# Kernel optimization log

Hardware: AMD Instinct MI355X
Metric: run time of the kernel (lower is better)

The kernel has to match this reference:

```python
import jax, jax.numpy as jnp
import numpy as np

STRIDE = (1, 1, 1)
PAD = (1, 1, 1)
CPG = 8  # channel_per_group


def setup_inputs() -> dict:
    key = jax.random.key(0)
    k1, k2, k3 = jax.random.split(key, 3)
    x = jax.random.normal(k1, (1, 64, 8, 56, 56), jnp.float32)
    offset = jax.random.normal(k2, (1, 648, 8, 56, 56), jnp.float32)
    n = 64 * 3 * 3 * 3
    stdv = 1.0 / np.sqrt(n)
    weight = jax.random.uniform(k3, (64, 64, 3, 3, 3), jnp.float32, -stdv, stdv)
    return {"x": x, "offset": offset, "weight": weight}


def _deform_conv3d(x, offset, weight, stride, padding, cpg):
    B, C, D, H, W = x.shape
    O, _, kD, kH, kW = weight.shape
    KV = kD * kH * kW
    G = C // cpg
    Do = (D + 2 * padding[0] - kD) // stride[0] + 1
    Ho = (H + 2 * padding[1] - kH) // stride[1] + 1
    Wo = (W + 2 * padding[2] - kW) // stride[2] + 1

    # offsets: [B, G, KV, 3(z,y,x), Do, Ho, Wo]
    off = offset.reshape(B, G, KV, 3, Do, Ho, Wo)

    f32 = x.dtype
    kz, ky, kx = jnp.meshgrid(jnp.arange(kD), jnp.arange(kH), jnp.arange(kW), indexing='ij')
    kz = kz.reshape(-1).astype(f32); ky = ky.reshape(-1).astype(f32); kx = kx.reshape(-1).astype(f32)
    oz = (jnp.arange(Do) * stride[0] - padding[0]).astype(f32)
    oy = (jnp.arange(Ho) * stride[1] - padding[1]).astype(f32)
    ox = (jnp.arange(Wo) * stride[2] - padding[2]).astype(f32)

    # sampling coords, broadcast to [B, G, KV, Do, Ho, Wo]
    zc = kz[None, None, :, None, None, None] + oz[None, None, None, :, None, None] + off[:, :, :, 0]
    yc = ky[None, None, :, None, None, None] + oy[None, None, None, None, :, None] + off[:, :, :, 1]
    xc = kx[None, None, :, None, None, None] + ox[None, None, None, None, None, :] + off[:, :, :, 2]

    z0 = jnp.floor(zc); y0 = jnp.floor(yc); x0 = jnp.floor(xc)
    dz = zc - z0; dy = yc - y0; dx = xc - x0
    z0i = z0.astype(jnp.int32); y0i = y0.astype(jnp.int32); x0i = x0.astype(jnp.int32)

    # channels-last grouped view: [B, G, D, H, W, cpg]
    xg = x.reshape(B, G, cpg, D, H, W).transpose(0, 1, 3, 4, 5, 2)
    bi = jnp.arange(B).reshape(B, 1, 1, 1, 1, 1)
    gi = jnp.arange(G).reshape(1, G, 1, 1, 1, 1)

    def gather(zi, yi, xi):
        valid = ((zi >= 0) & (zi < D) & (yi >= 0) & (yi < H) & (xi >= 0) & (xi < W))
        zcl = jnp.clip(zi, 0, D - 1)
        ycl = jnp.clip(yi, 0, H - 1)
        xcl = jnp.clip(xi, 0, W - 1)
        v = xg[bi, gi, zcl, ycl, xcl]  # [B,G,KV,Do,Ho,Wo,cpg]
        return v * valid.astype(f32)[..., None]

    val = jnp.zeros((B, G, KV, Do, Ho, Wo, cpg), f32)
    for zi, wz in ((z0i, 1.0 - dz), (z0i + 1, dz)):
        for yi, wy in ((y0i, 1.0 - dy), (y0i + 1, dy)):
            for xi, wx in ((x0i, 1.0 - dx), (x0i + 1, dx)):
                val = val + gather(zi, yi, xi) * (wz * wy * wx)[..., None]

    # [B,G,KV,Do,Ho,Wo,cpg] -> [B, C, KV, N]
    val = val.transpose(0, 1, 6, 2, 3, 4, 5).reshape(B, C, KV, Do * Ho * Wo)
    wmat = weight.reshape(O, C, KV)
    out = jnp.einsum('bckn,ock->bon', val, wmat)
    return out.reshape(B, O, Do, Ho, Wo)


def reference(x, offset, weight):
    return _deform_conv3d(x, offset, weight, STRIDE, PAD, CPG)
```

## Files before the change

kernel.cpp:

```cpp
#include <hip/hip_runtime.h>
#include <hip/hip_fp16.h>

namespace {
constexpr int D_ = 8, H_ = 56, W_ = 56;
constexpr int HW_ = H_ * W_;
constexpr int KV_ = 27;
constexpr int N_ = D_ * H_ * W_;
constexpr int NT_ = 16;
constexpr int NTILES_ = N_ / NT_;
}

typedef _Float16 f16x8 __attribute__((ext_vector_type(8)));
typedef float f32x4 __attribute__((ext_vector_type(4)));

union U4H { uint4 u; __half2 h[4]; f16x8 v; };

__global__ __launch_bounds__(256) void prep_kernel(const float* __restrict__ x,
                                                   const float* __restrict__ w,
                                                   __half* __restrict__ xt,
                                                   __half* __restrict__ wt2) {
    const int b = blockIdx.x, tid = threadIdx.x;
    if (b < 784) {
        const int g = b / 98;
        const int n = (b % 98) * 256 + tid;
        U4H p;
#pragma unroll
        for (int cc = 0; cc < 4; ++cc) {
            float lo = x[(size_t)(g * 8 + 2 * cc) * N_ + n];
            float hi = x[(size_t)(g * 8 + 2 * cc + 1) * N_ + n];
            p.h[cc] = __floats2half2_rn(lo, hi);
        }
        *(uint4*)(xt + ((size_t)g * N_ + n) * 8) = p.u;
    } else {
        const int idx = (b - 784) * 256 + tid;
        const int e  = idx & 7;
        const int l  = (idx >> 3) & 63;
        const int ks = (idx >> 9) & 1;
        const int of = (idx >> 10) & 3;
        const int kv = idx >> 12;
        const int o = of * 16 + (l & 15);
        const int c = ks * 32 + (l >> 4) * 8 + e;
        wt2[idx] = __float2half(w[(size_t)(o * 64 + c) * 27 + kv]);
    }
}

#define CORN(DU, WF, A) do {                                                   \
    U4H d_; d_.u = (DU);                                                       \
    __half2 w2_ = __float2half2_rn(WF);                                        \
    A.h[0] = __hfma2(d_.h[0], w2_, A.h[0]);                                    \
    A.h[1] = __hfma2(d_.h[1], w2_, A.h[1]);                                    \
    A.h[2] = __hfma2(d_.h[2], w2_, A.h[2]);                                    \
    A.h[3] = __hfma2(d_.h[3], w2_, A.h[3]);                                    \
} while (0)

__global__ __launch_bounds__(512, 4) void gather_kernel(const float* __restrict__ offset,
                                                        const __half* __restrict__ xt,
                                                        __half* __restrict__ val) {
    __shared__ uint4 lds_x[8 * 10 * 56];
    const int b2 = (blockIdx.x & 7) * 84 + (blockIdx.x >> 3);
    const int g = b2 / 84;
    const int r = b2 % 84;
    const int ys = (r / 3) * 2;
    const int kvt = r % 3;
    const int tid = threadIdx.x;

    const int ylo = max(0, ys - 4);
    const int yhi = min(55, ys + 5);
    const int Yw = yhi - ylo + 1;

    const uint4* xs = (const uint4*)(xt + (size_t)g * (N_ * 8));

    {
        const int tot = 8 * Yw * 56;
        for (int i = tid; i < tot; i += 512) {
            int z = i / (Yw * 56);
            int rem = i - z * (Yw * 56);
            int yy = rem / 56;
            int x = rem - yy * 56;
            lds_x[(z * 10 + yy) * 56 + x] = xs[z * HW_ + (ylo + yy) * 56 + x];
        }
    }
    __syncthreads();

    const float* obase = offset + (size_t)g * (KV_ * 3 * N_);
    const int kz = kvt;

    for (int s = tid; s < 8064; s += 512) {
        const int kvi = s / 896;
        const int p = s - kvi * 896;
        const int z = p / 112;
        const int rem = p - z * 112;
        const int yrow = rem / 56;
        const int x = rem - yrow * 56;
        const int y = ys + yrow;
        const int n = z * HW_ + y * W_ + x;
        const int kv = kvt * 9 + kvi;
        const int ky = kvi / 3, kx = kvi - ky * 3;

        const float* pofs = obase + (size_t)(kv * 3) * N_ + n;
        const float oz = __builtin_nontemporal_load(pofs);
        const float oy = __builtin_nontemporal_load(pofs + N_);
        const float ox = __builtin_nontemporal_load(pofs + 2 * N_);

        float zc = (float)(z + kz - 1) + oz;
        float yc = (float)(y + ky - 1) + oy;
        float xc = (float)(x + kx - 1) + ox;
        float zf = floorf(zc), yf = floorf(yc), xf = floorf(xc);
        float dz = zc - zf, dy = yc - yf, dx = xc - xf;
        int z0 = (int)zf, y0 = (int)yf, x0 = (int)xf;
        int z1 = z0 + 1, y1 = y0 + 1, x1 = x0 + 1;
        float wz0 = (1.f - dz) * ((unsigned)z0 < (unsigned)D_ ? 1.f : 0.f);
        float wz1 = dz * ((unsigned)z1 < (unsigned)D_ ? 1.f : 0.f);
        float wy0 = (1.f - dy) * ((unsigned)y0 < (unsigned)H_ ? 1.f : 0.f);
        float wy1 = dy * ((unsigned)y1 < (unsigned)H_ ? 1.f : 0.f);
        float wx0 = (1.f - dx) * ((unsigned)x0 < (unsigned)W_ ? 1.f : 0.f);
        float wx1 = dx * ((unsigned)x1 < (unsigned)W_ ? 1.f : 0.f);
        int z0c = min(max(z0, 0), D_ - 1), z1c = min(max(z1, 0), D_ - 1);
        int y0c = min(max(y0, 0), H_ - 1), y1c = min(max(y1, 0), H_ - 1);
        int x0c = min(max(x0, 0), W_ - 1), x1c = min(max(x1, 0), W_ - 1);

        uint4 c0, c1, c2, c3, c4, c5, c6, c7;
        const bool inw = (y0c >= ylo) && (y1c <= yhi);
        if (inw) {
            const int r00 = (z0c * 10 + (y0c - ylo)) * 56;
            const int r01 = (z0c * 10 + (y1c - ylo)) * 56;
            const int r10 = (z1c * 10 + (y0c - ylo)) * 56;
            const int r11 = (z1c * 10 + (y1c - ylo)) * 56;
            c0 = lds_x[r00 + x0c]; c1 = lds_x[r00 + x1c];
            c2 = lds_x[r01 + x0c]; c3 = lds_x[r01 + x1c];
            c4 = lds_x[r10 + x0c]; c5 = lds_x[r10 + x1c];
            c6 = lds_x[r11 + x0c]; c7 = lds_x[r11 + x1c];
        } else {
            const int zy00 = z0c * HW_ + y0c * W_, zy01 = z0c * HW_ + y1c * W_;
            const int zy10 = z1c * HW_ + y0c * W_, zy11 = z1c * HW_ + y1c * W_;
            c0 = xs[zy00 + x0c]; c1 = xs[zy00 + x1c];
            c2 = xs[zy01 + x0c]; c3 = xs[zy01 + x1c];
            c4 = xs[zy10 + x0c]; c5 = xs[zy10 + x1c];
            c6 = xs[zy11 + x0c]; c7 = xs[zy11 + x1c];
        }

        U4H a0, a1;
        a0.u = make_uint4(0u, 0u, 0u, 0u);
        a1.u = make_uint4(0u, 0u, 0u, 0u);
        float wzy00 = wz0 * wy0, wzy01 = wz0 * wy1;
        float wzy10 = wz1 * wy0, wzy11 = wz1 * wy1;
        CORN(c0, wzy00 * wx0, a0); CORN(c1, wzy00 * wx1, a1);
        CORN(c2, wzy01 * wx0, a0); CORN(c3, wzy01 * wx1, a1);
        CORN(c4, wzy10 * wx0, a0); CORN(c5, wzy10 * wx1, a1);
        CORN(c6, wzy11 * wx0, a0); CORN(c7, wzy11 * wx1, a1);
        a0.h[0] = __hadd2(a0.h[0], a1.h[0]);
        a0.h[1] = __hadd2(a0.h[1], a1.h[1]);
        a0.h[2] = __hadd2(a0.h[2], a1.h[2]);
        a0.h[3] = __hadd2(a0.h[3], a1.h[3]);

        const size_t didx = ((size_t)(kv * NTILES_ + (n >> 4)) << 10) + g * 128 + (n & 15) * 8;
        *(uint4*)(val + didx) = a0.u;
    }
}

__global__ __launch_bounds__(256, 4) void gemm_kernel(const __half* __restrict__ val,
                                                      const __half* __restrict__ wt2,
                                                      float* __restrict__ out) {
    __shared__ float red_s[4][64][20];
    const int tid = threadIdx.x, lane = tid & 63, wv = tid >> 6;
    const int nt = blockIdx.x;
    const int n0 = nt * NT_, nl = lane & 15;
    const int kv0 = wv * 7;
    f32x4 acc[4] = {};
    const __half* vb = val + (size_t)nt * 1024 + lane * 8;
    const __half* wb0 = wt2 + lane * 8;
#pragma unroll
    for (int t = 0; t < 7; ++t) {
        const int kv = kv0 + t;
        if (kv < KV_) {
            const __half* vp = vb + (size_t)kv * (NTILES_ * 1024);
            f16x8 bf0 = *(const f16x8*)(vp);
            f16x8 bf1 = *(const f16x8*)(vp + 512);
            const __half* wb = wb0 + (size_t)kv * 4096;
            f16x8 a00 = *(const f16x8*)(wb);
            f16x8 a01 = *(const f16x8*)(wb + 1024);
            f16x8 a02 = *(const f16x8*)(wb + 2048);
            f16x8 a03 = *(const f16x8*)(wb + 3072);
            acc[0] = __builtin_amdgcn_mfma_f32_16x16x32_f16(a00, bf0, acc[0], 0, 0, 0);
            acc[1] = __builtin_amdgcn_mfma_f32_16x16x32_f16(a01, bf0, acc[1], 0, 0, 0);
            acc[2] = __builtin_amdgcn_mfma_f32_16x16x32_f16(a02, bf0, acc[2], 0, 0, 0);
            acc[3] = __builtin_amdgcn_mfma_f32_16x16x32_f16(a03, bf0, acc[3], 0, 0, 0);
            f16x8 a10 = *(const f16x8*)(wb + 512);
            f16x8 a11 = *(const f16x8*)(wb + 1536);
            f16x8 a12 = *(const f16x8*)(wb + 2560);
            f16x8 a13 = *(const f16x8*)(wb + 3584);
            acc[0] = __builtin_amdgcn_mfma_f32_16x16x32_f16(a10, bf1, acc[0], 0, 0, 0);
            acc[1] = __builtin_amdgcn_mfma_f32_16x16x32_f16(a11, bf1, acc[1], 0, 0, 0);
            acc[2] = __builtin_amdgcn_mfma_f32_16x16x32_f16(a12, bf1, acc[2], 0, 0, 0);
            acc[3] = __builtin_amdgcn_mfma_f32_16x16x32_f16(a13, bf1, acc[3], 0, 0, 0);
        }
    }
#pragma unroll
    for (int of = 0; of < 4; ++of)
#pragma unroll
        for (int rr = 0; rr < 4; ++rr)
            red_s[wv][of * 16 + (lane >> 4) * 4 + rr][nl] = acc[of][rr];
    __syncthreads();
    const int o = tid >> 2, n4 = (tid & 3) * 4;
    f32x4 s = *(const f32x4*)&red_s[0][o][n4] + *(const f32x4*)&red_s[1][o][n4]
            + *(const f32x4*)&red_s[2][o][n4] + *(const f32x4*)&red_s[3][o][n4];
    *(f32x4*)(out + (size_t)o * N_ + n0 + n4) = s;
}

#define ISSUE(PH, KY, KX, OZ, OY, OX, BUF, WW) do {                            \
    float zc = (float)(zo + kz - 1) + (OZ);                                    \
    float yc = (float)(yo + (KY) - 1) + (OY);                                  \
    float xc = (float)(xo + (KX) - 1) + (OX);                                  \
    float zf = floorf(zc), yf = floorf(yc), xf = floorf(xc);                   \
    float dz = zc - zf, dy = yc - yf, dx = xc - xf;                            \
    int z0 = (int)zf, y0 = (int)yf, x0 = (int)xf;                              \
    int z1 = z0 + 1, y1 = y0 + 1, x1 = x0 + 1;                                 \
    WW[0] = (1.f - dz) * ((unsigned)z0 < (unsigned)D_ ? 1.f : 0.f);            \
    WW[1] = dz * ((unsigned)z1 < (unsigned)D_ ? 1.f : 0.f);                    \
    WW[2] = (1.f - dy) * ((unsigned)y0 < (unsigned)H_ ? 1.f : 0.f);            \
    WW[3] = dy * ((unsigned)y1 < (unsigned)H_ ? 1.f : 0.f);                    \
    WW[4] = (1.f - dx) * ((unsigned)x0 < (unsigned)W_ ? 1.f : 0.f);            \
    WW[5] = dx * ((unsigned)x1 < (unsigned)W_ ? 1.f : 0.f);                    \
    int z0c = min(max(z0, 0), D_ - 1), z1c = min(max(z1, 0), D_ - 1);          \
    int y0c = min(max(y0, 0), H_ - 1), y1c = min(max(y1, 0), H_ - 1);          \
    int x0c = min(max(x0, 0), W_ - 1), x1c = min(max(x1, 0), W_ - 1);          \
    const uint4* xp_ = xg[PH];                                                 \
    int zy00 = z0c * HW_ + y0c * W_, zy01 = z0c * HW_ + y1c * W_;              \
    int zy10 = z1c * HW_ + y0c * W_, zy11 = z1c * HW_ + y1c * W_;              \
    BUF[0] = xp_[zy00 + x0c]; BUF[1] = xp_[zy00 + x1c];                        \
    BUF[2] = xp_[zy01 + x0c]; BUF[3] = xp_[zy01 + x1c];                        \
    BUF[4] = xp_[zy10 + x0c]; BUF[5] = xp_[zy10 + x1c];                        \
    BUF[6] = xp_[zy11 + x0c]; BUF[7] = xp_[zy11 + x1c];                        \
} while (0)

#define CONSUME(BUF, WW, BF) do {                                              \
    U4H a0_, a1_;                                                              \
    a0_.u = make_uint4(0u, 0u, 0u, 0u);                                        \
    a1_.u = make_uint4(0u, 0u, 0u, 0u);                                        \
    float wzy00 = WW[0] * WW[2], wzy01 = WW[0] * WW[3];                        \
    float wzy10 = WW[1] * WW[2], wzy11 = WW[1] * WW[3];                        \
    CORN(BUF[0], wzy00 * WW[4], a0_); CORN(BUF[1], wzy00 * WW[5], a1_);        \
    CORN(BUF[2], wzy01 * WW[4], a0_); CORN(BUF[3], wzy01 * WW[5], a1_);        \
    CORN(BUF[4], wzy10 * WW[4], a0_); CORN(BUF[5], wzy10 * WW[5], a1_);        \
    CORN(BUF[6], wzy11 * WW[4], a0_); CORN(BUF[7], wzy11 * WW[5], a1_);        \
    a0_.h[0] = __hadd2(a0_.h[0], a1_.h[0]);                                    \
    a0_.h[1] = __hadd2(a0_.h[1], a1_.h[1]);                                    \
    a0_.h[2] = __hadd2(a0_.h[2], a1_.h[2]);                                    \
    a0_.h[3] = __hadd2(a0_.h[3], a1_.h[3]);                                    \
    BF = a0_.v;                                                                \
} while (0)

__global__ __launch_bounds__(192, 3) void dconv_kernel(const float* __restrict__ offset,
                                                       const __half* __restrict__ xt,
                                                       const __half* __restrict__ wt2,
                                                       float* __restrict__ out) {
    __shared__ float red_s[3][64][20];
    const int tid = threadIdx.x;
    const int lane = tid & 63;
    const int wv = tid >> 6;
    const int r = blockIdx.x;
    const int tile = (r & 7) * 196 + (r >> 3);
    const int n0 = tile * NT_;
    const int nl = lane & 15;
    const int n = n0 + nl;
    const int kv0 = wv * 9;
    const int kz = wv;

    const int zo = n / HW_;
    const int rem = n - zo * HW_;
    const int yo = rem / W_;
    const int xo = rem - yo * W_;
    const uint4* xg[2];
    const float* ob[2];
#pragma unroll
    for (int ph = 0; ph < 2; ++ph) {
        const int g = ph * 4 + (lane >> 4);
        xg[ph] = (const uint4*)(xt + (size_t)g * (N_ * 8));
        ob[ph] = offset + (size_t)g * (KV_ * 3 * N_) + n;
    }

    uint4 bufA[8], bufB[8];
    float wA[6], wB[6];
    f32x4 acc[4] = {};
    f16x8 bf0, bf1;

    float o0z[2], o0y[2], o0x[2], onz[2], ony[2], onx[2];
#pragma unroll
    for (int ph = 0; ph < 2; ++ph) {
        const float* p = ob[ph] + (size_t)kv0 * 3 * N_;
        o0z[ph] = __builtin_nontemporal_load(p);
        o0y[ph] = __builtin_nontemporal_load(p + N_);
        o0x[ph] = __builtin_nontemporal_load(p + 2 * N_);
    }
    ISSUE(0, 0, 0, o0z[0], o0y[0], o0x[0], bufA, wA);
    ISSUE(1, 0, 0, o0z[1], o0y[1], o0x[1], bufB, wB);
#pragma unroll
    for (int ph = 0; ph < 2; ++ph) {
        const float* p = ob[ph] + (size_t)(kv0 + 1) * 3 * N_;
        onz[ph] = __builtin_nontemporal_load(p);
        ony[ph] = __builtin_nontemporal_load(p + N_);
        onx[ph] = __builtin_nontemporal_load(p + 2 * N_);
    }

#pragma unroll
    for (int t = 0; t < 9; ++t) {
        const int kv = kv0 + t;
        const __half* wb = wt2 + (size_t)kv * 4096 + lane * 8;
        f16x8 af00 = *(const f16x8*)(wb);
        f16x8 af01 = *(const f16x8*)(wb + 1024);
        f16x8 af02 = *(const f16x8*)(wb + 2048);
        f16x8 af03 = *(const f16x8*)(wb + 3072);
        CONSUME(bufA, wA, bf0);
        if (t < 8)
            ISSUE(0, (t + 1) / 3, (t + 1) % 3, onz[0], ony[0], onx[0], bufA, wA);
        __builtin_amdgcn_s_setprio(1);
        acc[0] = __builtin_amdgcn_mfma_f32_16x16x32_f16(af00, bf0, acc[0], 0, 0, 0);
        acc[1] = __builtin_amdgcn_mfma_f32_16x16x32_f16(af01, bf0, acc[1], 0, 0, 0);
        acc[2] = __builtin_amdgcn_mfma_f32_16x16x32_f16(af02, bf0, acc[2], 0, 0, 0);
        acc[3] = __builtin_amdgcn_mfma_f32_16x16x32_f16(af03, bf0, acc[3], 0, 0, 0);
        __builtin_amdgcn_s_setprio(0);
        f16x8 af10 = *(const f16x8*)(wb + 512);
        f16x8 af11 = *(const f16x8*)(wb + 1536);
        f16x8 af12 = *(const f16x8*)(wb + 2560);
        f16x8 af13 = *(const f16x8*)(wb + 3584);
        CONSUME(bufB, wB, bf1);
        if (t < 8)
            ISSUE(1, (t + 1) / 3, (t + 1) % 3, onz[1], ony[1], onx[1], bufB, wB);
        float tnz[2], tny[2], tnx[2];
        if (t < 7) {
#pragma unroll
            for (int ph = 0; ph < 2; ++ph) {
                const float* p = ob[ph] + (size_t)(kv + 2) * 3 * N_;
                tnz[ph] = __builtin_nontemporal_load(p);
                tny[ph] = __builtin_nontemporal_load(p + N_);
                tnx[ph] = __builtin_nontemporal_load(p + 2 * N_);
            }
        }
        __builtin_amdgcn_s_setprio(1);
        acc[0] = __builtin_amdgcn_mfma_f32_16x16x32_f16(af10, bf1, acc[0], 0, 0, 0);
        acc[1] = __builtin_amdgcn_mfma_f32_16x16x32_f16(af11, bf1, acc[1], 0, 0, 0);
        acc[2] = __builtin_amdgcn_mfma_f32_16x16x32_f16(af12, bf1, acc[2], 0, 0, 0);
        acc[3] = __builtin_amdgcn_mfma_f32_16x16x32_f16(af13, bf1, acc[3], 0, 0, 0);
        __builtin_amdgcn_s_setprio(0);
        if (t < 7) {
#pragma unroll
            for (int ph = 0; ph < 2; ++ph) {
                onz[ph] = tnz[ph]; ony[ph] = tny[ph]; onx[ph] = tnx[ph];
            }
        }
    }

#pragma unroll
    for (int of = 0; of < 4; ++of)
#pragma unroll
        for (int rr = 0; rr < 4; ++rr)
            red_s[wv][of * 16 + (lane >> 4) * 4 + rr][nl] = acc[of][rr];
    __syncthreads();
    for (int e = tid; e < 256; e += 192) {
        const int o = e >> 2, n4 = (e & 3) * 4;
        f32x4 s = *(const f32x4*)&red_s[0][o][n4]
                + *(const f32x4*)&red_s[1][o][n4]
                + *(const f32x4*)&red_s[2][o][n4];
        *(f32x4*)(out + (size_t)o * N_ + n0 + n4) = s;
    }
}

extern "C" void kernel_launch(void* const* d_in, const int* in_sizes, int n_in,
                              void* d_out, int out_size, void* d_ws, size_t ws_size,
                              hipStream_t stream) {
    const float* x      = (const float*)d_in[0];
    const float* offset = (const float*)d_in[1];
    const float* weight = (const float*)d_in[2];
    float* out = (float*)d_out;

    __half* xt  = (__half*)d_ws;
    __half* wt2 = xt + (size_t)8 * N_ * 8;
    const size_t base = 3432448;
    const size_t val_bytes = (size_t)KV_ * NTILES_ * 1024 * 2;

    prep_kernel<<<784 + 432, 256, 0, stream>>>(x, weight, xt, wt2);

    if (ws_size >= base + val_bytes) {
        __half* val = (__half*)((char*)d_ws + base);
        gather_kernel<<<672, 512, 0, stream>>>(offset, xt, val);
        gemm_kernel<<<NTILES_, 256, 0, stream>>>(val, wt2, out);
    } else {
        dconv_kernel<<<NTILES_, 192, 0, stream>>>(offset, xt, wt2, out);
    }
}
```

Measured before the change: 173.5 us.

## Tile gather kernel along x to shrink LDS window and raise occupancy

The gather kernel now splits each y-pair/kz block further into three x-strips, so the shared-memory halo window shrinks from 56 to at most 28 columns. The grid grows from 672 to 2016 blocks and launch bounds request 8 blocks per CU, aiming for more parallelism and occupancy on the offset-load-bound gather. The reduced window makes more samples fall outside it and take the global-memory fallback, and the halo columns are loaded redundantly across neighbouring strips. In the GEMM kernel, all weight fragment loads are hoisted ahead of the MFMAs and the MFMA block is wrapped in s_setprio to favour matrix issue.

```diff
diff --git a/kernel.cpp b/kernel.cpp
--- a/kernel.cpp
+++ b/kernel.cpp
@@ -53,17 +53,25 @@
     A.h[3] = __hfma2(d_.h[3], w2_, A.h[3]);                                    \
 } while (0)
 
-__global__ __launch_bounds__(512, 4) void gather_kernel(const float* __restrict__ offset,
+__global__ __launch_bounds__(512, 8) void gather_kernel(const float* __restrict__ offset,
                                                         const __half* __restrict__ xt,
                                                         __half* __restrict__ val) {
-    __shared__ uint4 lds_x[8 * 10 * 56];
-    const int b2 = (blockIdx.x & 7) * 84 + (blockIdx.x >> 3);
-    const int g = b2 / 84;
-    const int r = b2 % 84;
-    const int ys = (r / 3) * 2;
-    const int kvt = r % 3;
+    __shared__ uint4 lds_x[8 * 10 * 28];
+    const int bid = blockIdx.x;
+    const int g = bid & 7;
+    const int r = bid >> 3;
+    const int yp = r / 9;
+    const int rr = r - yp * 9;
+    const int kzp = rr / 3;
+    const int xt3 = rr - kzp * 3;
     const int tid = threadIdx.x;
 
+    const int ys = yp * 2;
+    const int xbase = xt3 * 19;
+    const int xw = (xt3 == 2) ? 18 : 19;
+    const int xlo = max(0, xbase - 4);
+    const int xhi = min(55, xbase + xw + 4);
+    const int XW = xhi - xlo + 1;
     const int ylo = max(0, ys - 4);
     const int yhi = min(55, ys + 5);
     const int Yw = yhi - ylo + 1;
@@ -71,30 +79,32 @@
     const uint4* xs = (const uint4*)(xt + (size_t)g * (N_ * 8));
 
     {
-        const int tot = 8 * Yw * 56;
+        const int tot = 8 * Yw * XW;
         for (int i = tid; i < tot; i += 512) {
-            int z = i / (Yw * 56);
-            int rem = i - z * (Yw * 56);
-            int yy = rem / 56;
-            int x = rem - yy * 56;
-            lds_x[(z * 10 + yy) * 56 + x] = xs[z * HW_ + (ylo + yy) * 56 + x];
+            int z = i / (Yw * XW);
+            int rem = i - z * (Yw * XW);
+            int yy = rem / XW;
+            int xx = rem - yy * XW;
+            lds_x[(z * 10 + yy) * 28 + xx] = xs[z * HW_ + (ylo + yy) * W_ + (xlo + xx)];
         }
     }
     __syncthreads();
 
     const float* obase = offset + (size_t)g * (KV_ * 3 * N_);
-    const int kz = kvt;
-
-    for (int s = tid; s < 8064; s += 512) {
-        const int kvi = s / 896;
-        const int p = s - kvi * 896;
-        const int z = p / 112;
-        const int rem = p - z * 112;
-        const int yrow = rem / 56;
-        const int x = rem - yrow * 56;
+    const int kz = kzp;
+    const int tot_s = 9 * 8 * 2 * xw;
+
+    for (int s = tid; s < tot_s; s += 512) {
+        const int t1 = s / xw;
+        const int xi = s - t1 * xw;
+        const int yrow = t1 & 1;
+        const int t2 = t1 >> 1;
+        const int z = t2 & 7;
+        const int kvi = t2 >> 3;
+        const int x = xbase + xi;
         const int y = ys + yrow;
         const int n = z * HW_ + y * W_ + x;
-        const int kv = kvt * 9 + kvi;
+        const int kv = kzp * 9 + kvi;
         const int ky = kvi / 3, kx = kvi - ky * 3;
 
         const float* pofs = obase + (size_t)(kv * 3) * N_ + n;
@@ -120,16 +130,18 @@
         int x0c = min(max(x0, 0), W_ - 1), x1c = min(max(x1, 0), W_ - 1);
 
         uint4 c0, c1, c2, c3, c4, c5, c6, c7;
-        const bool inw = (y0c >= ylo) && (y1c <= yhi);
+        const bool inw = (y0c >= ylo) & (y1c <= yhi) & (x0c >= xlo) & (x1c <= xhi);
         if (inw) {
-            const int r00 = (z0c * 10 + (y0c - ylo)) * 56;
-            const int r01 = (z0c * 10 + (y1c - ylo)) * 56;
-            const int r10 = (z1c * 10 + (y0c - ylo)) * 56;
-            const int r11 = (z1c * 10 + (y1c - ylo)) * 56;
-            c0 = lds_x[r00 + x0c]; c1 = lds_x[r00 + x1c];
-            c2 = lds_x[r01 + x0c]; c3 = lds_x[r01 + x1c];
-            c4 = lds_x[r10 + x0c]; c5 = lds_x[r10 + x1c];
-            c6 = lds_x[r11 + x0c]; c7 = lds_x[r11 + x1c];
+            const int ya = y0c - ylo, yb = y1c - ylo;
+            const int xa = x0c - xlo, xb = x1c - xlo;
+            const int r00 = (z0c * 10 + ya) * 28;
+            const int r01 = (z0c * 10 + yb) * 28;
+            const int r10 = (z1c * 10 + ya) * 28;
+            const int r11 = (z1c * 10 + yb) * 28;
+            c0 = lds_x[r00 + xa]; c1 = lds_x[r00 + xb];
+            c2 = lds_x[r01 + xa]; c3 = lds_x[r01 + xb];
+            c4 = lds_x[r10 + xa]; c5 = lds_x[r10 + xb];
+            c6 = lds_x[r11 + xa]; c7 = lds_x[r11 + xb];
         } else {
             const int zy00 = z0c * HW_ + y0c * W_, zy01 = z0c * HW_ + y1c * W_;
             const int zy10 = z1c * HW_ + y0c * W_, zy11 = z1c * HW_ + y1c * W_;
@@ -181,18 +193,20 @@
             f16x8 a01 = *(const f16x8*)(wb + 1024);
             f16x8 a02 = *(const f16x8*)(wb + 2048);
             f16x8 a03 = *(const f16x8*)(wb + 3072);
+            f16x8 a10 = *(const f16x8*)(wb + 512);
+            f16x8 a11 = *(const f16x8*)(wb + 1536);
+            f16x8 a12 = *(const f16x8*)(wb + 2560);
+            f16x8 a13 = *(const f16x8*)(wb + 3584);
+            __builtin_amdgcn_s_setprio(1);
             acc[0] = __builtin_amdgcn_mfma_f32_16x16x32_f16(a00, bf0, acc[0], 0, 0, 0);
             acc[1] = __builtin_amdgcn_mfma_f32_16x16x32_f16(a01, bf0, acc[1], 0, 0, 0);
             acc[2] = __builtin_amdgcn_mfma_f32_16x16x32_f16(a02, bf0, acc[2], 0, 0, 0);
             acc[3] = __builtin_amdgcn_mfma_f32_16x16x32_f16(a03, bf0, acc[3], 0, 0, 0);
-            f16x8 a10 = *(const f16x8*)(wb + 512);
-            f16x8 a11 = *(const f16x8*)(wb + 1536);
-            f16x8 a12 = *(const f16x8*)(wb + 2560);
-            f16x8 a13 = *(const f16x8*)(wb + 3584);
             acc[0] = __builtin_amdgcn_mfma_f32_16x16x32_f16(a10, bf1, acc[0], 0, 0, 0);
             acc[1] = __builtin_amdgcn_mfma_f32_16x16x32_f16(a11, bf1, acc[1], 0, 0, 0);
             acc[2] = __builtin_amdgcn_mfma_f32_16x16x32_f16(a12, bf1, acc[2], 0, 0, 0);
             acc[3] = __builtin_amdgcn_mfma_f32_16x16x32_f16(a13, bf1, acc[3], 0, 0, 0);
+            __builtin_amdgcn_s_setprio(0);
         }
     }
 #pragma unroll
@@ -382,7 +396,7 @@
 
     if (ws_size >= base + val_bytes) {
         __half* val = (__half*)((char*)d_ws + base);
-        gather_kernel<<<672, 512, 0, stream>>>(offset, xt, val);
+        gather_kernel<<<2016, 512, 0, stream>>>(offset, xt, val);
         gemm_kernel<<<NTILES_, 256, 0, stream>>>(val, wt2, out);
     } else {
         dconv_kernel<<<NTILES_, 192, 0, stream>>>(offset, xt, wt2, out);
```

Result: no change. 171.5 us (-1.1%).
